# Performance work log

Measured on AMD Instinct MI355X. Metric: run time of the kernel, lower is better.

## Reference

```python
import jax, jax.numpy as jnp
import numpy as np

N_NODES = 50000
N_EDGES = 1600000
D_IN = 64
D_OUT = 64
N_REL = 6


def setup_inputs() -> dict:
    key = jax.random.key(0)
    k = jax.random.split(key, 6)
    x = jax.random.normal(k[0], (N_NODES, D_IN), dtype=jnp.float32)
    edge_index = jax.random.randint(k[1], (2, N_EDGES), 0, N_NODES, dtype=jnp.int32)
    edge_type = jax.random.randint(k[2], (N_EDGES,), 0, N_REL, dtype=jnp.int32)
    # RGCN parameters: per-relation weight, root (self-loop) weight, bias
    W = jax.random.normal(k[3], (N_REL, D_IN, D_OUT), dtype=jnp.float32) / np.float32(np.sqrt(D_IN))
    root = jax.random.normal(k[4], (D_IN, D_OUT), dtype=jnp.float32) / np.float32(np.sqrt(D_IN))
    bias = jnp.zeros((D_OUT,), dtype=jnp.float32)
    return {"x": x, "W": W, "root": root, "bias": bias,
            "edge_index": edge_index, "edge_type": edge_type}


def reference(x, W, root, bias, edge_index, edge_type):
    """RGCNConv forward (PyG semantics, default aggr='mean' per relation):
    out[i] = bias + x[i] @ root + sum_r mean_{j in N_r(i)} (x[j] @ W_r)
    """
    src, dst = edge_index[0], edge_index[1]
    # Transform all node features by all relation weights: [R, N, D_OUT]
    xr = jnp.einsum('nd,rdo->rno', x, W)
    # Per-edge message: relation-specific transformed source feature [E, D_OUT]
    m = xr[edge_type, src]
    # Mean normalization per (dst node, relation): 1 / #relation-r in-edges of dst
    seg = dst.astype(jnp.int32) * N_REL + edge_type.astype(jnp.int32)
    count = jax.ops.segment_sum(jnp.ones((m.shape[0],), x.dtype), seg,
                                num_segments=N_NODES * N_REL)
    norm = jnp.where(count > 0, 1.0 / jnp.maximum(count, 1.0), 0.0)
    m = m * norm[seg][:, None]
    # Scatter-add aggregation over destination nodes
    agg = jax.ops.segment_sum(m, dst, num_segments=N_NODES)
    return agg + x @ root + bias
```

## Files before the change

### kernel.cpp

```cpp
#include <hip/hip_runtime.h>

#define NN 50000
#define NE 1600000
#define D 64
#define NR 6
#define NSEG (NN * NR)
#define SB 512
#define BFRAG_N (4 * 14 * 64 * 8)
#define EPB 6400
#define NBLK1 (NE / EPB)
#define BUKSH 9
#define NBUK ((NSEG + 511) >> 9)
#define NG (NBUK * NBLK1)
#define SNB1 ((NG + SB - 1) / SB)
#define PREPB ((NN * D / 8 + 255) / 256)

typedef __attribute__((ext_vector_type(8))) short short8;
typedef __attribute__((ext_vector_type(4))) float f32x4;

__device__ __forceinline__ unsigned short f2bf(float f) {
    unsigned int u = __float_as_uint(f);
    unsigned int r = (u + 0x7FFF + ((u >> 16) & 1)) >> 16;
    return (unsigned short)r;
}

__global__ __launch_bounds__(256) void prep_hist_k(const float* __restrict__ x,
                                                   const float* __restrict__ W,
                                                   const float* __restrict__ root,
                                                   const int* __restrict__ dsts,
                                                   const int* __restrict__ et,
                                                   int* __restrict__ ghist,
                                                   unsigned short* __restrict__ xh,
                                                   unsigned short* __restrict__ Bfrag) {
    __shared__ int lh[NBUK];
    int tid = threadIdx.x;
    if (blockIdx.x < NBLK1) {
        int blk = blockIdx.x;
        for (int i = tid; i < NBUK; i += 256) lh[i] = 0;
        __syncthreads();
        int base = blk * EPB;
#pragma unroll 5
        for (int i = 0; i < EPB / 256; ++i) {
            int e = base + i * 256 + tid;
            int seg = dsts[e] * NR + et[e];
            atomicAdd(&lh[seg >> BUKSH], 1);
        }
        __syncthreads();
        for (int i = tid; i < NBUK; i += 256) ghist[i * NBLK1 + blk] = lh[i];
    } else {
        int t = (blockIdx.x - NBLK1) * 256 + tid;
        if (t < NN * D / 8) {
            const float4* xp = (const float4*)(x + (size_t)t * 8);
            float4 va = xp[0], vb = xp[1];
            uint4 o;
            o.x = (unsigned int)f2bf(va.x) | ((unsigned int)f2bf(va.y) << 16);
            o.y = (unsigned int)f2bf(va.z) | ((unsigned int)f2bf(va.w) << 16);
            o.z = (unsigned int)f2bf(vb.x) | ((unsigned int)f2bf(vb.y) << 16);
            o.w = (unsigned int)f2bf(vb.z) | ((unsigned int)f2bf(vb.w) << 16);
            *(uint4*)(xh + (size_t)t * 8) = o;
        }
        if (t < BFRAG_N) {
            int j = t & 7;
            int lane = (t >> 3) & 63;
            int rest = t >> 9;
            int ks = rest % 14;
            int nt = rest / 14;
            int k = ks * 32 + ((lane >> 4) * 8) + j;
            int n = nt * 16 + (lane & 15);
            float v = (k < 384) ? W[(size_t)k * 64 + n] : root[(size_t)(k - 384) * 64 + n];
            Bfrag[t] = f2bf(v);
        }
    }
}

__global__ void scanA_k(const int* __restrict__ v, int* __restrict__ incl,
                        int* __restrict__ blocksum, int n) {
    __shared__ int s[SB];
    int t = threadIdx.x, i = blockIdx.x * SB + t;
    s[t] = (i < n) ? v[i] : 0;
    __syncthreads();
    for (int off = 1; off < SB; off <<= 1) {
        int u = (t >= off) ? s[t - off] : 0;
        __syncthreads();
        s[t] += u;
        __syncthreads();
    }
    if (i < n) incl[i] = s[t];
    if (t == SB - 1) blocksum[blockIdx.x] = s[t];
}

__global__ void scanB_k(const int* __restrict__ blocksum, int* __restrict__ blockoff, int nb) {
    __shared__ int s[1024];
    int t = threadIdx.x;
    s[t] = (t < nb) ? blocksum[t] : 0;
    __syncthreads();
    for (int off = 1; off < 1024; off <<= 1) {
        int u = (t >= off) ? s[t - off] : 0;
        __syncthreads();
        s[t] += u;
        __syncthreads();
    }
    if (t < nb) blockoff[t] = s[t];
}

__global__ void scanC2_k(const int* __restrict__ incl, const int* __restrict__ blockoff,
                         const int* __restrict__ v, int* __restrict__ excl, int n) {
    int i = blockIdx.x * blockDim.x + threadIdx.x;
    if (i >= n) return;
    int b = i / SB;
    int Ri = incl[i] + (b > 0 ? blockoff[b - 1] : 0);
    excl[i] = Ri - v[i];
}

__global__ __launch_bounds__(256) void scatter1_k(const int* __restrict__ srcs,
                                                  const int* __restrict__ dsts,
                                                  const int* __restrict__ et,
                                                  const int* __restrict__ goff,
                                                  unsigned int* __restrict__ kv) {
    __shared__ int cur[NBUK];
    int tid = threadIdx.x, blk = blockIdx.x;
    for (int i = tid; i < NBUK; i += 256) cur[i] = goff[i * NBLK1 + blk];
    __syncthreads();
    int base = blk * EPB;
#pragma unroll 5
    for (int i = 0; i < EPB / 256; ++i) {
        int e = base + i * 256 + tid;
        int seg = dsts[e] * NR + et[e];
        int pos = atomicAdd(&cur[seg >> BUKSH], 1);
        kv[pos] = ((unsigned int)srcs[e] << BUKSH) | ((unsigned int)seg & 511u);
    }
}

__global__ __launch_bounds__(256) void bucket2_k(const unsigned int* __restrict__ kv,
                                                 const int* __restrict__ goff,
                                                 int* __restrict__ rowstart,
                                                 unsigned short* __restrict__ pay) {
    __shared__ int h[512];
    __shared__ int part[256];
    int tid = threadIdx.x, b = blockIdx.x;
    int base = goff[b * NBLK1];
    int end  = (b + 1 < NBUK) ? goff[(b + 1) * NBLK1] : NE;
    for (int i = tid; i < 512; i += 256) h[i] = 0;
    __syncthreads();
    for (int k = base + tid; k < end; k += 256)
        atomicAdd(&h[kv[k] & 511u], 1);
    __syncthreads();
    int c0 = h[2 * tid], c1 = h[2 * tid + 1];
    part[tid] = c0 + c1;
    __syncthreads();
    for (int off = 1; off < 256; off <<= 1) {
        int u = (tid >= off) ? part[tid - off] : 0;
        __syncthreads();
        part[tid] += u;
        __syncthreads();
    }
    int pbase = (tid > 0) ? part[tid - 1] : 0;
    __syncthreads();
    int e0 = pbase, e1 = pbase + c0;
    h[2 * tid] = e0; h[2 * tid + 1] = e1;
    int segb = b << BUKSH;
    if (segb + 2 * tid     < NSEG) rowstart[segb + 2 * tid]     = base + e0;
    if (segb + 2 * tid + 1 < NSEG) rowstart[segb + 2 * tid + 1] = base + e1;
    if (b == 0 && tid == 0) rowstart[NSEG] = NE;
    __syncthreads();
    for (int k = base + tid; k < end; k += 256) {
        unsigned int v = kv[k];
        int pos = base + atomicAdd(&h[v & 511u], 1);
        pay[pos] = (unsigned short)(v >> BUKSH);
    }
}

__global__ __launch_bounds__(256) void agg13_k(const unsigned short* __restrict__ xh,
                                               const int* __restrict__ rowstart,
                                               const unsigned short* __restrict__ pay,
                                               unsigned short* __restrict__ Amain) {
    int wv = (blockIdx.x * blockDim.x + threadIdx.x) >> 6;
    int lane = threadIdx.x & 63;
    int g = lane >> 3;
    int q = lane & 7;
    int seg = 8 * wv + g;
    int k0 = rowstart[seg], k1 = rowstart[seg + 1];
    const char* xb = (const char*)xh;
    unsigned int qo = (unsigned int)q << 4;
    float a0 = 0.f, a1 = 0.f, a2 = 0.f, a3 = 0.f;
    float a4 = 0.f, a5 = 0.f, a6 = 0.f, a7 = 0.f;
    int len = k1 - k0;
    int k = k0;
    int k4 = k0 + (len & ~3);
    for (; k < k4; k += 4) {
        unsigned int pv[4];
#pragma unroll
        for (int j = 0; j < 4; ++j) pv[j] = (unsigned int)pay[k + j] << 7;
        uint4 uv[4];
#pragma unroll
        for (int j = 0; j < 4; ++j)
            uv[j] = *(const uint4*)(xb + pv[j] + qo);
#pragma unroll
        for (int j = 0; j < 4; ++j) {
            a0 += __uint_as_float(uv[j].x << 16);
            a1 += __uint_as_float(uv[j].x & 0xFFFF0000u);
            a2 += __uint_as_float(uv[j].y << 16);
            a3 += __uint_as_float(uv[j].y & 0xFFFF0000u);
            a4 += __uint_as_float(uv[j].z << 16);
            a5 += __uint_as_float(uv[j].z & 0xFFFF0000u);
            a6 += __uint_as_float(uv[j].w << 16);
            a7 += __uint_as_float(uv[j].w & 0xFFFF0000u);
        }
    }
    if (k < k1) {
        unsigned int pv[3];
        float mv[3];
#pragma unroll
        for (int j = 0; j < 3; ++j) {
            int kk = k + j;
            bool v = kk < k1;
            mv[j] = v ? 1.0f : 0.0f;
            pv[j] = (unsigned int)pay[v ? kk : k] << 7;
        }
#pragma unroll
        for (int j = 0; j < 3; ++j) {
            uint4 u = *(const uint4*)(xb + pv[j] + qo);
            a0 += __uint_as_float(u.x << 16) * mv[j];
            a1 += __uint_as_float(u.x & 0xFFFF0000u) * mv[j];
            a2 += __uint_as_float(u.y << 16) * mv[j];
            a3 += __uint_as_float(u.y & 0xFFFF0000u) * mv[j];
            a4 += __uint_as_float(u.z << 16) * mv[j];
            a5 += __uint_as_float(u.z & 0xFFFF0000u) * mv[j];
            a6 += __uint_as_float(u.w << 16) * mv[j];
            a7 += __uint_as_float(u.w & 0xFFFF0000u) * mv[j];
        }
    }
    float nrm = (len > 0) ? 1.0f / (float)len : 0.0f;
    uint4 o;
    o.x = (unsigned int)f2bf(a0 * nrm) | ((unsigned int)f2bf(a1 * nrm) << 16);
    o.y = (unsigned int)f2bf(a2 * nrm) | ((unsigned int)f2bf(a3 * nrm) << 16);
    o.z = (unsigned int)f2bf(a4 * nrm) | ((unsigned int)f2bf(a5 * nrm) << 16);
    o.w = (unsigned int)f2bf(a6 * nrm) | ((unsigned int)f2bf(a7 * nrm) << 16);
    *(uint4*)((char*)Amain + (size_t)seg * 128 + qo) = o;
}

__global__ __launch_bounds__(256) void mix4_k(const unsigned short* __restrict__ Amain,
                                              const unsigned short* __restrict__ xh,
                                              const unsigned short* __restrict__ Bfrag,
                                              const float* __restrict__ bias,
                                              float* __restrict__ out) {
    int t = threadIdx.x;
    int lane = t & 63;
    int w = t >> 6;
    int rowb = blockIdx.x * 64 + w * 16;
    int arow = rowb + (lane & 15);
    if (arow >= NN) arow = NN - 1;
    int ko = (lane >> 4) * 8;
    const unsigned short* ap = Amain + (size_t)arow * 384 + ko;
    const unsigned short* xp = xh + (size_t)arow * 64 + ko;
    const short8* bp = (const short8*)Bfrag + lane;
    f32x4 acc0 = {0.f, 0.f, 0.f, 0.f};
    f32x4 acc1 = acc0, acc2 = acc0, acc3 = acc0;
#pragma unroll
    for (int ks = 0; ks < 14; ++ks) {
        short8 a = (ks < 12) ? *(const short8*)(ap + ks * 32)
                             : *(const short8*)(xp + (ks - 12) * 32);
        short8 b0 = bp[(0 * 14 + ks) * 64];
        short8 b1 = bp[(1 * 14 + ks) * 64];
        short8 b2 = bp[(2 * 14 + ks) * 64];
        short8 b3 = bp[(3 * 14 + ks) * 64];
        acc0 = __builtin_amdgcn_mfma_f32_16x16x32_bf16(a, b0, acc0, 0, 0, 0);
        acc1 = __builtin_amdgcn_mfma_f32_16x16x32_bf16(a, b1, acc1, 0, 0, 0);
        acc2 = __builtin_amdgcn_mfma_f32_16x16x32_bf16(a, b2, acc2, 0, 0, 0);
        acc3 = __builtin_amdgcn_mfma_f32_16x16x32_bf16(a, b3, acc3, 0, 0, 0);
    }
    int col = lane & 15;
    int rout = rowb + (lane >> 4) * 4;
    float bv0 = bias[0 * 16 + col];
    float bv1 = bias[1 * 16 + col];
    float bv2 = bias[2 * 16 + col];
    float bv3 = bias[3 * 16 + col];
#pragma unroll
    for (int j = 0; j < 4; ++j) {
        int rr = rout + j;
        if (rr < NN) {
            float* op = out + (size_t)rr * 64;
            op[0 * 16 + col] = acc0[j] + bv0;
            op[1 * 16 + col] = acc1[j] + bv1;
            op[2 * 16 + col] = acc2[j] + bv2;
            op[3 * 16 + col] = acc3[j] + bv3;
        }
    }
}

__global__ void zero_i32_k(int* __restrict__ p, int n) {
    int i = blockIdx.x * blockDim.x + threadIdx.x;
    if (i < n) p[i] = 0;
}

__global__ void count_edges_k(const int* __restrict__ dst, const int* __restrict__ et,
                              int* __restrict__ cnt) {
    int e = blockIdx.x * blockDim.x + threadIdx.x;
    if (e < NE) atomicAdd(&cnt[dst[e] * NR + et[e]], 1);
}

__global__ void make_norm_k(const int* __restrict__ cnt, float* __restrict__ norm, int n) {
    int i = blockIdx.x * blockDim.x + threadIdx.x;
    if (i < n) {
        int c = cnt[i];
        norm[i] = (c > 0) ? 1.0f / (float)c : 0.0f;
    }
}

__global__ void init_out_k(const float* __restrict__ x, const float* __restrict__ root,
                           const float* __restrict__ bias, float* __restrict__ out) {
    int t = blockIdx.x * blockDim.x + threadIdx.x;
    int n = t >> 6;
    int o = t & 63;
    if (n >= NN) return;
    const float* xrow = x + n * D;
    float acc = bias[o];
#pragma unroll
    for (int d = 0; d < D; ++d) acc = fmaf(xrow[d], root[d * D + o], acc);
    out[t] = acc;
}

__global__ void scatter_mv_k(const int* __restrict__ srcs, const int* __restrict__ dsts,
                             const int* __restrict__ et, const float* __restrict__ x,
                             const float* __restrict__ W, const float* __restrict__ norm,
                             float* __restrict__ out) {
    int t = blockIdx.x * blockDim.x + threadIdx.x;
    int e = t >> 6;
    int o = t & 63;
    if (e >= NE) return;
    int s = srcs[e];
    int d2 = dsts[e];
    int r = et[e];
    float nrm = norm[d2 * NR + r];
    const float* xrow = x + s * D;
    const float* Wr = W + r * D * D + o;
    float acc = 0.0f;
#pragma unroll
    for (int d = 0; d < D; ++d) acc = fmaf(xrow[d], Wr[d * D], acc);
    atomicAdd(&out[d2 * D + o], acc * nrm);
}

extern "C" void kernel_launch(void* const* d_in, const int* in_sizes, int n_in,
                              void* d_out, int out_size, void* d_ws, size_t ws_size,
                              hipStream_t stream) {
    const float* x    = (const float*)d_in[0];
    const float* W    = (const float*)d_in[1];
    const float* root = (const float*)d_in[2];
    const float* bias = (const float*)d_in[3];
    const int*   ei   = (const int*)d_in[4];
    const int*   et   = (const int*)d_in[5];
    float* out = (float*)d_out;
    const int* srcs = ei;
    const int* dsts = ei + NE;

    char* ws = (char*)d_ws;
    size_t off = 0;
    int*   rowstart = (int*)(ws + off); off += (size_t)(NSEG + 1) * 4;
    off = (off + 255) & ~(size_t)255;
    unsigned short* pay = (unsigned short*)(ws + off); off += (size_t)NE * 2;
    off = (off + 255) & ~(size_t)255;
    unsigned int* kv = (unsigned int*)(ws + off); off += (size_t)NE * 4;
    int*   ghist    = (int*)(ws + off); off += (size_t)NG * 4;
    int*   incl     = (int*)(ws + off); off += (size_t)NG * 4;
    int*   goff     = (int*)(ws + off); off += (size_t)NG * 4;
    int*   blocksum = (int*)(ws + off); off += (size_t)SNB1 * 4;
    int*   blockoff = (int*)(ws + off); off += (size_t)SNB1 * 4;
    off = (off + 255) & ~(size_t)255;
    unsigned short* Bfrag = (unsigned short*)(ws + off); off += (size_t)BFRAG_N * 2;
    off = (off + 255) & ~(size_t)255;
    unsigned short* xh = (unsigned short*)(ws + off); off += (size_t)NN * D * 2;
    off = (off + 255) & ~(size_t)255;
    unsigned short* Amain = (unsigned short*)(ws + off); off += (size_t)NN * 384 * 2;
    bool big = ws_size >= off;

    if (big) {
        prep_hist_k<<<NBLK1 + PREPB, 256, 0, stream>>>(x, W, root, dsts, et, ghist, xh, Bfrag);
        scanA_k<<<SNB1, SB, 0, stream>>>(ghist, incl, blocksum, NG);
        scanB_k<<<1, 1024, 0, stream>>>(blocksum, blockoff, SNB1);
        scanC2_k<<<(NG + 255) / 256, 256, 0, stream>>>(incl, blockoff, ghist, goff, NG);
        scatter1_k<<<NBLK1, 256, 0, stream>>>(srcs, dsts, et, goff, kv);
        bucket2_k<<<NBUK, 256, 0, stream>>>(kv, goff, rowstart, pay);
        int aggwaves = NSEG / 8;
        agg13_k<<<((size_t)aggwaves * 64 + 255) / 256, 256, 0, stream>>>(xh, rowstart, pay, Amain);
        mix4_k<<<(NN + 63) / 64, 256, 0, stream>>>(Amain, xh, Bfrag, bias, out);
    } else {
        int* cnt2  = (int*)(ws);
        float* norm = (float*)(ws + (size_t)NSEG * 4);
        zero_i32_k<<<(NSEG + 255) / 256, 256, 0, stream>>>(cnt2, NSEG);
        count_edges_k<<<(NE + 255) / 256, 256, 0, stream>>>(dsts, et, cnt2);
        make_norm_k<<<(NSEG + 255) / 256, 256, 0, stream>>>(cnt2, norm, NSEG);
        init_out_k<<<((size_t)NN * 64 + 255) / 256, 256, 0, stream>>>(x, root, bias, out);
        scatter_mv_k<<<((size_t)NE * 64 + 255) / 256, 256, 0, stream>>>(srcs, dsts, et, x, W, norm, out);
    }
}
```

Before: 95.36 us.

## Fold scan finalization into consumers and stage bucket keys in LDS

Removes the scanC2 kernel and its goff array; scatter1 and bucket2 now compute the exclusive offsets on the fly from the inclusive scan, the block offsets and the histogram. bucket2 also copies each bucket's keys into a 16KB shared buffer once, so the histogram and placement passes read from LDS rather than reading global memory twice. This saves one launch plus one global read pass, in exchange for a larger LDS footprint in bucket2 that may lower occupancy, and a fallback to global reads for buckets with more than 4096 entries.

```diff
diff --git a/kernel.cpp b/kernel.cpp
--- a/kernel.cpp
+++ b/kernel.cpp
@@ -14,6 +14,7 @@
 #define NG (NBUK * NBLK1)
 #define SNB1 ((NG + SB - 1) / SB)
 #define PREPB ((NN * D / 8 + 255) / 256)
+#define KVL_CAP 4096
 
 typedef __attribute__((ext_vector_type(8))) short short8;
 typedef __attribute__((ext_vector_type(4))) float f32x4;
@@ -22,6 +23,13 @@
     unsigned int u = __float_as_uint(f);
     unsigned int r = (u + 0x7FFF + ((u >> 16) & 1)) >> 16;
     return (unsigned short)r;
+}
+
+__device__ __forceinline__ int excl_at(const int* __restrict__ incl,
+                                       const int* __restrict__ blockoff,
+                                       const int* __restrict__ ghist, int m) {
+    int bo = (m >= SB) ? blockoff[m / SB - 1] : 0;
+    return incl[m] + bo - ghist[m];
 }
 
 __global__ __launch_bounds__(256) void prep_hist_k(const float* __restrict__ x,
@@ -103,23 +111,19 @@
     if (t < nb) blockoff[t] = s[t];
 }
 
-__global__ void scanC2_k(const int* __restrict__ incl, const int* __restrict__ blockoff,
-                         const int* __restrict__ v, int* __restrict__ excl, int n) {
-    int i = blockIdx.x * blockDim.x + threadIdx.x;
-    if (i >= n) return;
-    int b = i / SB;
-    int Ri = incl[i] + (b > 0 ? blockoff[b - 1] : 0);
-    excl[i] = Ri - v[i];
-}
-
 __global__ __launch_bounds__(256) void scatter1_k(const int* __restrict__ srcs,
                                                   const int* __restrict__ dsts,
                                                   const int* __restrict__ et,
-                                                  const int* __restrict__ goff,
+                                                  const int* __restrict__ incl,
+                                                  const int* __restrict__ blockoff,
+                                                  const int* __restrict__ ghist,
                                                   unsigned int* __restrict__ kv) {
     __shared__ int cur[NBUK];
     int tid = threadIdx.x, blk = blockIdx.x;
-    for (int i = tid; i < NBUK; i += 256) cur[i] = goff[i * NBLK1 + blk];
+    for (int i = tid; i < NBUK; i += 256) {
+        int m = i * NBLK1 + blk;
+        cur[i] = excl_at(incl, blockoff, ghist, m);
+    }
     __syncthreads();
     int base = blk * EPB;
 #pragma unroll 5
@@ -132,18 +136,33 @@
 }
 
 __global__ __launch_bounds__(256) void bucket2_k(const unsigned int* __restrict__ kv,
-                                                 const int* __restrict__ goff,
+                                                 const int* __restrict__ incl,
+                                                 const int* __restrict__ blockoff,
+                                                 const int* __restrict__ ghist,
                                                  int* __restrict__ rowstart,
                                                  unsigned short* __restrict__ pay) {
     __shared__ int h[512];
     __shared__ int part[256];
+    __shared__ unsigned int kvl[KVL_CAP];
+    __shared__ int sbase, send;
     int tid = threadIdx.x, b = blockIdx.x;
-    int base = goff[b * NBLK1];
-    int end  = (b + 1 < NBUK) ? goff[(b + 1) * NBLK1] : NE;
+    if (tid == 0) {
+        sbase = excl_at(incl, blockoff, ghist, b * NBLK1);
+        send = (b + 1 < NBUK) ? excl_at(incl, blockoff, ghist, (b + 1) * NBLK1) : NE;
+    }
     for (int i = tid; i < 512; i += 256) h[i] = 0;
     __syncthreads();
-    for (int k = base + tid; k < end; k += 256)
-        atomicAdd(&h[kv[k] & 511u], 1);
+    int base = sbase, end = send;
+    int cnt = end - base;
+    bool inlds = (cnt <= KVL_CAP);
+    if (inlds) {
+        for (int k = tid; k < cnt; k += 256) kvl[k] = kv[base + k];
+    }
+    __syncthreads();
+    for (int k = tid; k < cnt; k += 256) {
+        unsigned int v = inlds ? kvl[k] : kv[base + k];
+        atomicAdd(&h[v & 511u], 1);
+    }
     __syncthreads();
     int c0 = h[2 * tid], c1 = h[2 * tid + 1];
     part[tid] = c0 + c1;
@@ -163,8 +182,8 @@
     if (segb + 2 * tid + 1 < NSEG) rowstart[segb + 2 * tid + 1] = base + e1;
     if (b == 0 && tid == 0) rowstart[NSEG] = NE;
     __syncthreads();
-    for (int k = base + tid; k < end; k += 256) {
-        unsigned int v = kv[k];
+    for (int k = tid; k < cnt; k += 256) {
+        unsigned int v = inlds ? kvl[k] : kv[base + k];
         int pos = base + atomicAdd(&h[v & 511u], 1);
         pay[pos] = (unsigned short)(v >> BUKSH);
     }
@@ -362,7 +381,6 @@
     unsigned int* kv = (unsigned int*)(ws + off); off += (size_t)NE * 4;
     int*   ghist    = (int*)(ws + off); off += (size_t)NG * 4;
     int*   incl     = (int*)(ws + off); off += (size_t)NG * 4;
-    int*   goff     = (int*)(ws + off); off += (size_t)NG * 4;
     int*   blocksum = (int*)(ws + off); off += (size_t)SNB1 * 4;
     int*   blockoff = (int*)(ws + off); off += (size_t)SNB1 * 4;
     off = (off + 255) & ~(size_t)255;
@@ -377,9 +395,8 @@
         prep_hist_k<<<NBLK1 + PREPB, 256, 0, stream>>>(x, W, root, dsts, et, ghist, xh, Bfrag);
         scanA_k<<<SNB1, SB, 0, stream>>>(ghist, incl, blocksum, NG);
         scanB_k<<<1, 1024, 0, stream>>>(blocksum, blockoff, SNB1);
-        scanC2_k<<<(NG + 255) / 256, 256, 0, stream>>>(incl, blockoff, ghist, goff, NG);
-        scatter1_k<<<NBLK1, 256, 0, stream>>>(srcs, dsts, et, goff, kv);
-        bucket2_k<<<NBUK, 256, 0, stream>>>(kv, goff, rowstart, pay);
+        scatter1_k<<<NBLK1, 256, 0, stream>>>(srcs, dsts, et, incl, blockoff, ghist, kv);
+        bucket2_k<<<NBUK, 256, 0, stream>>>(kv, incl, blockoff, ghist, rowstart, pay);
         int aggwaves = NSEG / 8;
         agg13_k<<<((size_t)aggwaves * 64 + 255) / 256, 256, 0, stream>>>(xh, rowstart, pay, Amain);
         mix4_k<<<(NN + 63) / 64, 256, 0, stream>>>(Amain, xh, Bfrag, bias, out);
```

Result: no change. 94.82 us (-0.6%).
